# Performance work log

Hardware: AMD Instinct MI355X
Metric: run time of the kernel (lower is better)

The kernel has to match this reference:

```python
import jax, jax.numpy as jnp
import numpy as np

EMBED_DIM = 1024
N_HEADS = 16
HEAD_DIM = EMBED_DIM // N_HEADS


def setup_inputs() -> dict:
    key = jax.random.key(0)
    ks = jax.random.split(key, 9)
    s = 1.0 / np.sqrt(EMBED_DIM)
    x = jax.random.normal(ks[0], (4, 2048, EMBED_DIM), dtype=jnp.float32)
    Wq = jax.random.uniform(ks[1], (EMBED_DIM, EMBED_DIM), jnp.float32, -s, s)
    bq = jax.random.uniform(ks[2], (EMBED_DIM,), jnp.float32, -s, s)
    Wk = jax.random.uniform(ks[3], (EMBED_DIM, EMBED_DIM), jnp.float32, -s, s)
    bk = jax.random.uniform(ks[4], (EMBED_DIM,), jnp.float32, -s, s)
    Wv = jax.random.uniform(ks[5], (EMBED_DIM, EMBED_DIM), jnp.float32, -s, s)
    bv = jax.random.uniform(ks[6], (EMBED_DIM,), jnp.float32, -s, s)
    Wo = jax.random.uniform(ks[7], (EMBED_DIM, EMBED_DIM), jnp.float32, -s, s)
    bo = jax.random.uniform(ks[8], (EMBED_DIM,), jnp.float32, -s, s)
    return {"x": x, "Wq": Wq, "bq": bq, "Wk": Wk, "bk": bk,
            "Wv": Wv, "bv": bv, "Wo": Wo, "bo": bo}


def reference(x, Wq, bq, Wk, bk, Wv, bv, Wo, bo):
    B, S, _ = x.shape
    # projections (PyTorch Linear: x @ W.T + b; weights stored as [in,out] here)
    q = x @ Wq + bq
    k = x @ Wk + bk
    v = x @ Wv + bv
    # [B, H, S, D]
    q = q.reshape(B, S, N_HEADS, HEAD_DIM).transpose(0, 2, 1, 3)
    k = k.reshape(B, S, N_HEADS, HEAD_DIM).transpose(0, 2, 1, 3)
    v = v.reshape(B, S, N_HEADS, HEAD_DIM).transpose(0, 2, 1, 3)
    scores = jnp.einsum('bhsd,bhtd->bhst', q, k) / np.sqrt(HEAD_DIM).astype(np.float32)
    attn = jax.nn.softmax(scores, axis=-1)
    out = jnp.einsum('bhst,bhtd->bhsd', attn, v)
    out = out.transpose(0, 2, 1, 3).reshape(B, S, EMBED_DIM)
    return out @ Wo + bo  # dropout=0 (eval) -> identity
```

## Files before the change

### kernel.cpp

```cpp
#include <hip/hip_runtime.h>
#include <stdint.h>

#define EMBED 1024
#define NH 16
#define HD 64
#define SEQ 2048
#define BATCH 4
#define M_TOT (BATCH*SEQ)
#define QSCALE 0.18033688011112042f

typedef __attribute__((ext_vector_type(8))) short short8;
typedef __attribute__((ext_vector_type(4))) float floatx4;
typedef __attribute__((ext_vector_type(4))) unsigned int uintx4;

__device__ __forceinline__ unsigned short f2bf(float f) {
    union { float f; unsigned int u; } v; v.f = f;
    unsigned int r = v.u + 0x7fffu + ((v.u >> 16) & 1u);
    return (unsigned short)(r >> 16);
}

__device__ __forceinline__ void load_lds16(const unsigned short* g, unsigned short* l) {
    __builtin_amdgcn_global_load_lds(
        (const __attribute__((address_space(1))) unsigned int*)g,
        (__attribute__((address_space(3))) unsigned int*)l, 16, 0, 0);
}

__global__ void cvt_x(const float* __restrict__ x, unsigned short* __restrict__ xb) {
    int i = (blockIdx.x * 256 + threadIdx.x) * 4;
    float4 v = *(const float4*)(x + i);
    ushort4 o;
    o.x = f2bf(v.x); o.y = f2bf(v.y); o.z = f2bf(v.z); o.w = f2bf(v.w);
    *(ushort4*)(xb + i) = o;
}

__global__ void wtrans(const float* __restrict__ w0, const float* __restrict__ w1,
                       const float* __restrict__ w2, const float* __restrict__ w3,
                       unsigned short* __restrict__ t0, unsigned short* __restrict__ t1,
                       unsigned short* __restrict__ t2, unsigned short* __restrict__ t3) {
    __shared__ float tile[32][33];
    const float* W; unsigned short* T;
    switch (blockIdx.z) { case 0: W=w0; T=t0; break; case 1: W=w1; T=t1; break;
                          case 2: W=w2; T=t2; break; default: W=w3; T=t3; }
    int n0 = blockIdx.x * 32, k0 = blockIdx.y * 32;
    int tx = threadIdx.x, ty = threadIdx.y;
    #pragma unroll
    for (int i = 0; i < 4; i++)
        tile[ty + i*8][tx] = W[(k0 + ty + i*8) * EMBED + n0 + tx];
    __syncthreads();
    #pragma unroll
    for (int i = 0; i < 4; i++)
        T[(n0 + ty + i*8) * EMBED + k0 + tx] = f2bf(tile[tx][ty + i*8]);
}

__global__ __launch_bounds__(256) void gemm_st(
        const unsigned short* __restrict__ A, const unsigned short* __restrict__ BT,
        const float* __restrict__ b0, const float* __restrict__ b1, const float* __restrict__ b2,
        void* __restrict__ o0, void* __restrict__ o1, void* __restrict__ o2, int mode) {
    __shared__ unsigned short As[128*32];
    __shared__ unsigned short Bs[128*32];
    int tid = threadIdx.x;
    int lane = tid & 63, wave = tid >> 6;
    int quad = lane >> 4, l16 = lane & 15;
    int id = blockIdx.x;
    int xcd = id & 7, j = id >> 3;
    int mblk = (xcd * 8 + (j & 7)) * 128;
    int nblk = (j >> 3) * 128;
    int wm = wave >> 1, wn = wave & 1;
    floatx4 acc[4][4];
    #pragma unroll
    for (int mt=0;mt<4;mt++)
      #pragma unroll
      for (int nt=0;nt<4;nt++)
        acc[mt][nt] = (floatx4){0.f,0.f,0.f,0.f};
    int lr = lane >> 2;
    int lc = ((lane & 3) ^ ((lr >> 1) & 3)) * 8;
    const unsigned short* Ag = A  + (size_t)(mblk + wave*32 + lr) * EMBED + lc;
    const unsigned short* Bg = BT + (size_t)(nblk + wave*32 + lr) * EMBED + lc;
    unsigned short* Asw = As + wave*1024;
    unsigned short* Bsw = Bs + wave*1024;
    int sa = (quad ^ ((l16 >> 1) & 3)) * 8;

    for (int k0 = 0; k0 < EMBED; k0 += 32) {
        load_lds16(Ag + k0,             Asw);
        load_lds16(Ag + 16*EMBED + k0,  Asw + 512);
        load_lds16(Bg + k0,             Bsw);
        load_lds16(Bg + 16*EMBED + k0,  Bsw + 512);
        __syncthreads();
        short8 af[4], bf[4];
        #pragma unroll
        for (int i=0;i<4;i++) {
            af[i] = *(const short8*)(As + (wm*64 + i*16 + l16)*32 + sa);
            bf[i] = *(const short8*)(Bs + (wn*64 + i*16 + l16)*32 + sa);
        }
        #pragma unroll
        for (int mt=0;mt<4;mt++)
          #pragma unroll
          for (int nt=0;nt<4;nt++)
            acc[mt][nt] = __builtin_amdgcn_mfma_f32_16x16x32_bf16(af[mt], bf[nt], acc[mt][nt], 0, 0, 0);
        __syncthreads();
    }
    if (mode == 1) {
        float* O = (float*)o0;
        #pragma unroll
        for (int mt=0;mt<4;mt++)
          #pragma unroll
          for (int nt=0;nt<4;nt++) {
            int col = nblk + wn*64 + nt*16 + l16;
            float bv = b0[col];
            #pragma unroll
            for (int r=0;r<4;r++) {
                int row = mblk + wm*64 + mt*16 + quad*4 + r;
                O[(size_t)row * EMBED + col] = acc[mt][nt][r] + bv;
            }
          }
    } else {
        int which = (nblk + wn*64) >> 10;
        const float* bs = (which==0) ? b0 : (which==1) ? b1 : b2;
        unsigned short* O = (unsigned short*)((which==0) ? o0 : (which==1) ? o1 : o2);
        #pragma unroll
        for (int mt=0;mt<4;mt++)
          #pragma unroll
          for (int nt=0;nt<4;nt++) {
            int coll = ((nblk + wn*64) & 1023) + nt*16 + l16;
            float bv = bs[coll];
            int h = coll >> 6, d = coll & 63;
            #pragma unroll
            for (int r=0;r<4;r++) {
                int row = mblk + wm*64 + mt*16 + quad*4 + r;
                int b = row >> 11, s = row & 2047;
                float v = acc[mt][nt][r] + bv;
                if (which == 0) {
                    v *= QSCALE;
                    O[((size_t)(b*NH + h)*SEQ + s)*HD + d] = f2bf(v);
                } else if (which == 1) {
                    O[((size_t)(b*NH + h)*SEQ + s)*HD + d] = f2bf(v);
                } else {
                    int sp = (s & ~31) | (((s >> 2) & 3) << 3) | (((s >> 4) & 1) << 2) | (s & 3);
                    O[((size_t)(b*NH + h)*HD + d)*SEQ + sp] = f2bf(v);
                }
            }
          }
    }
}

__global__ __launch_bounds__(512, 4) void attn(
    const unsigned short* __restrict__ Q, const unsigned short* __restrict__ K,
    const unsigned short* __restrict__ VTp, unsigned short* __restrict__ O) {
    __shared__ unsigned short kv[4096];
    int tid = threadIdx.x;
    int lane = tid & 63, wave = tid >> 6;
    int quad = lane >> 4, l16 = lane & 15;
    int id = blockIdx.x;
    int bh = (id & 7) * 8 + (id >> 6);
    int qblk = (id >> 3) & 7;
    int b = bh >> 4, h = bh & 15;
    int q0 = qblk * 256 + wave * 32;
    const unsigned short* Qb = Q + (size_t)bh * SEQ * HD;
    const unsigned short* Kb = K + (size_t)bh * SEQ * HD;
    const unsigned short* Vb = VTp + (size_t)bh * HD * SEQ;
    int li = (wave & 3) * 64 + lane;
    const unsigned short* src;
    unsigned short* dst = kv + (wave & 3) * 512 + ((wave >> 2) ? 2048 : 0);
    int src_step;
    if (wave < 4) {
        int t = li >> 3, slot = li & 7;
        int dblk = slot ^ (t & 7);
        src = Kb + (size_t)t * HD + dblk * 8;
        src_step = 32 * HD;
    } else {
        int d = li >> 2, slot = li & 3;
        int swz = (d & 3) ^ ((d >> 2) & 3);
        src = Vb + (size_t)d * SEQ + (slot ^ swz) * 8;
        src_step = 32;
    }
    short8 qf[2][2];
    #pragma unroll
    for (int mt=0;mt<2;mt++) {
        const unsigned short* qp = Qb + (size_t)(q0 + mt*16 + l16) * HD + quad*8;
        qf[mt][0] = *(const short8*)(qp);
        qf[mt][1] = *(const short8*)(qp + 32);
    }
    floatx4 o_acc[2][4], l_acc[2];
    #pragma unroll
    for (int mt=0;mt<2;mt++) {
        l_acc[mt] = (floatx4){0.f,0.f,0.f,0.f};
        #pragma unroll
        for (int dt=0;dt<4;dt++) o_acc[mt][dt] = (floatx4){0.f,0.f,0.f,0.f};
    }
    short8 ones;
    #pragma unroll
    for (int j=0;j<8;j++) ones[j] = (short)0x3F80;
    int koff[2][2], voff[4];
    #pragma unroll
    for (int nt=0;nt<2;nt++) {
        int t = nt*16 + l16;
        #pragma unroll
        for (int hh=0;hh<2;hh++)
            koff[nt][hh] = t*64 + ((hh*4 + quad) ^ (t & 7)) * 8;
    }
    #pragma unroll
    for (int dt=0;dt<4;dt++) {
        int d = dt*16 + l16;
        voff[dt] = 2048 + d*32 + ((quad ^ (d & 3) ^ ((d >> 2) & 3))) * 8;
    }

    for (int tb = 0; tb < SEQ; tb += 32) {
        load_lds16(src, dst);
        src += src_step;
        __syncthreads();
        short8 kf[2][2], vf[4];
        #pragma unroll
        for (int nt=0;nt<2;nt++) {
            kf[nt][0] = *(const short8*)(kv + koff[nt][0]);
            kf[nt][1] = *(const short8*)(kv + koff[nt][1]);
        }
        #pragma unroll
        for (int dt=0;dt<4;dt++)
            vf[dt] = *(const short8*)(kv + voff[dt]);
        floatx4 sacc[2][2];
        #pragma unroll
        for (int nt=0;nt<2;nt++)
          #pragma unroll
          for (int mt=0;mt<2;mt++) {
            floatx4 s = (floatx4){0.f,0.f,0.f,0.f};
            s = __builtin_amdgcn_mfma_f32_16x16x32_bf16(kf[nt][0], qf[mt][0], s, 0, 0, 0);
            s = __builtin_amdgcn_mfma_f32_16x16x32_bf16(kf[nt][1], qf[mt][1], s, 0, 0, 0);
            sacc[nt][mt] = s;
          }
        short8 pf[2];
        #pragma unroll
        for (int mt=0;mt<2;mt++) {
            uintx4 pu;
            #pragma unroll
            for (int jp=0;jp<4;jp++) {
                int nt = jp >> 1, rp = (jp & 1) * 2;
                union { float f; unsigned int u; } e0, e1;
                e0.f = __builtin_amdgcn_exp2f(sacc[nt][mt][rp]);
                e1.f = __builtin_amdgcn_exp2f(sacc[nt][mt][rp+1]);
                pu[jp] = ((e1.u + 0x8000u) & 0xFFFF0000u) | ((e0.u + 0x8000u) >> 16);
            }
            pf[mt] = __builtin_bit_cast(short8, pu);
        }
        #pragma unroll
        for (int mt=0;mt<2;mt++) {
            l_acc[mt] = __builtin_amdgcn_mfma_f32_16x16x32_bf16(ones, pf[mt], l_acc[mt], 0, 0, 0);
            #pragma unroll
            for (int dt=0;dt<4;dt++)
                o_acc[mt][dt] = __builtin_amdgcn_mfma_f32_16x16x32_bf16(vf[dt], pf[mt], o_acc[mt][dt], 0, 0, 0);
        }
        __syncthreads();
    }
    #pragma unroll
    for (int mt=0;mt<2;mt++) {
        float inv = 1.f / l_acc[mt][0];
        int s = q0 + mt*16 + l16;
        #pragma unroll
        for (int dt=0;dt<4;dt++) {
            ushort4 w;
            w.x = f2bf(o_acc[mt][dt][0]*inv);
            w.y = f2bf(o_acc[mt][dt][1]*inv);
            w.z = f2bf(o_acc[mt][dt][2]*inv);
            w.w = f2bf(o_acc[mt][dt][3]*inv);
            *(ushort4*)(O + ((size_t)b*SEQ + s)*EMBED + h*HD + dt*16 + quad*4) = w;
        }
    }
}

extern "C" void kernel_launch(void* const* d_in, const int* in_sizes, int n_in,
                              void* d_out, int out_size, void* d_ws, size_t ws_size,
                              hipStream_t stream) {
    const float* x  = (const float*)d_in[0];
    const float* Wq = (const float*)d_in[1]; const float* bq = (const float*)d_in[2];
    const float* Wk = (const float*)d_in[3]; const float* bk = (const float*)d_in[4];
    const float* Wv = (const float*)d_in[5]; const float* bv = (const float*)d_in[6];
    const float* Wo = (const float*)d_in[7]; const float* bo = (const float*)d_in[8];
    char* ws = (char*)d_ws;
    unsigned short* xb  = (unsigned short*)(ws);
    unsigned short* WqT = (unsigned short*)(ws + (16ull<<20));
    unsigned short* WkT = (unsigned short*)(ws + (18ull<<20));
    unsigned short* WvT = (unsigned short*)(ws + (20ull<<20));
    unsigned short* WoT = (unsigned short*)(ws + (22ull<<20));
    unsigned short* Qb  = (unsigned short*)(ws + (24ull<<20));
    unsigned short* Kb  = (unsigned short*)(ws + (40ull<<20));
    unsigned short* VTb = (unsigned short*)(ws + (56ull<<20));
    unsigned short* Ob  = xb;

    cvt_x<<<(M_TOT*EMBED)/1024, 256, 0, stream>>>(x, xb);
    wtrans<<<dim3(32,32,4), dim3(32,8), 0, stream>>>(Wq,Wk,Wv,Wo, WqT,WkT,WvT,WoT);
    gemm_st<<<dim3(1536), 256, 0, stream>>>(xb, WqT, bq, bk, bv, Qb, Kb, VTb, 0);
    attn<<<dim3(512), 512, 0, stream>>>(Qb, Kb, VTb, Ob);
    gemm_st<<<dim3(512), 256, 0, stream>>>(Ob, WoT, bo, bo, bo, (float*)d_out, nullptr, nullptr, 1);
}
```

Baseline: 289.6 us.

## Replace projection GEMM with 256x256 double-buffered eight-wave pipelined kernel

```diff
diff --git a/kernel.cpp b/kernel.cpp
--- a/kernel.cpp
+++ b/kernel.cpp
@@ -52,81 +52,164 @@
         T[(n0 + ty + i*8) * EMBED + k0 + tx] = f2bf(tile[tx][ty + i*8]);
 }
 
-__global__ __launch_bounds__(256) void gemm_st(
+#define ST_A(buf_, kt_) do { \
+    const unsigned short* s_ = Asrc + (kt_)*64; \
+    unsigned short* d_ = ldst + (buf_)*32768; \
+    load_lds16(s_,              d_); \
+    load_lds16(s_ + 64*EMBED,   d_ + 4096); \
+    load_lds16(s_ + 128*EMBED,  d_ + 8192); \
+    load_lds16(s_ + 192*EMBED,  d_ + 12288); \
+  } while(0)
+#define ST_B(buf_, kt_, h_) do { \
+    const unsigned short* s_ = Bsrc + (kt_)*64 + (h_)*128*EMBED; \
+    unsigned short* d_ = ldst + (buf_)*32768 + 16384 + (h_)*8192; \
+    load_lds16(s_,              d_); \
+    load_lds16(s_ + 64*EMBED,   d_ + 4096); \
+  } while(0)
+
+__global__ __launch_bounds__(512, 2) void gemm8(
         const unsigned short* __restrict__ A, const unsigned short* __restrict__ BT,
         const float* __restrict__ b0, const float* __restrict__ b1, const float* __restrict__ b2,
         void* __restrict__ o0, void* __restrict__ o1, void* __restrict__ o2, int mode) {
-    __shared__ unsigned short As[128*32];
-    __shared__ unsigned short Bs[128*32];
-    int tid = threadIdx.x;
-    int lane = tid & 63, wave = tid >> 6;
-    int quad = lane >> 4, l16 = lane & 15;
-    int id = blockIdx.x;
-    int xcd = id & 7, j = id >> 3;
-    int mblk = (xcd * 8 + (j & 7)) * 128;
-    int nblk = (j >> 3) * 128;
-    int wm = wave >> 1, wn = wave & 1;
-    floatx4 acc[4][4];
-    #pragma unroll
-    for (int mt=0;mt<4;mt++)
+    __shared__ unsigned short lds[2][2][256*64];
+    const int tid = threadIdx.x;
+    const int lane = tid & 63, wave = tid >> 6;
+    const int quad = lane >> 4, l16 = lane & 15;
+    const int wm = wave >> 2, wn = wave & 3;
+    const int id = blockIdx.x;
+    const int xcd = id & 7, j = id >> 3;
+    const int mblk = (xcd * 4 + (j & 3)) * 256;
+    const int nblk = (j >> 2) * 256;
+
+    const int srow = tid >> 3;
+    const int scol = ((tid & 7) ^ (srow & 7)) * 8;
+    const unsigned short* Asrc = A  + (size_t)(mblk + srow) * EMBED + scol;
+    const unsigned short* Bsrc = BT + (size_t)(nblk + srow) * EMBED + scol;
+    unsigned short* ldst = &lds[0][0][0] + wave * 512;
+
+    const int cs0 = ( quad      ^ (l16 & 7)) * 8;
+    const int cs1 = ((quad ^ 4) ^ (l16 & 7)) * 8;
+    const unsigned short* Abase = &lds[0][0][0] + (wm*128 + l16)*64;
+    const unsigned short* Bbase = &lds[0][1][0] + (wn*64  + l16)*64;
+
+    floatx4 acc[8][4];
+    #pragma unroll
+    for (int m=0;m<8;m++)
       #pragma unroll
-      for (int nt=0;nt<4;nt++)
-        acc[mt][nt] = (floatx4){0.f,0.f,0.f,0.f};
-    int lr = lane >> 2;
-    int lc = ((lane & 3) ^ ((lr >> 1) & 3)) * 8;
-    const unsigned short* Ag = A  + (size_t)(mblk + wave*32 + lr) * EMBED + lc;
-    const unsigned short* Bg = BT + (size_t)(nblk + wave*32 + lr) * EMBED + lc;
-    unsigned short* Asw = As + wave*1024;
-    unsigned short* Bsw = Bs + wave*1024;
-    int sa = (quad ^ ((l16 >> 1) & 3)) * 8;
-
-    for (int k0 = 0; k0 < EMBED; k0 += 32) {
-        load_lds16(Ag + k0,             Asw);
-        load_lds16(Ag + 16*EMBED + k0,  Asw + 512);
-        load_lds16(Bg + k0,             Bsw);
-        load_lds16(Bg + 16*EMBED + k0,  Bsw + 512);
-        __syncthreads();
-        short8 af[4], bf[4];
+      for (int n=0;n<4;n++) acc[m][n] = (floatx4){0.f,0.f,0.f,0.f};
+
+    ST_A(0,0); ST_B(0,0,0); ST_B(0,0,1);
+    ST_A(1,1);
+    asm volatile("s_waitcnt vmcnt(4)" ::: "memory");
+    __builtin_amdgcn_s_barrier();
+
+    #pragma unroll 2
+    for (int t = 0; t < 16; ++t) {
+        const int buf = t & 1;
+        const unsigned short* Ab = Abase + buf*32768;
+        const unsigned short* Bb = Bbase + buf*32768;
+        short8 fA[4][2], fBlo[2][2], fBhi[2][2];
         #pragma unroll
         for (int i=0;i<4;i++) {
-            af[i] = *(const short8*)(As + (wm*64 + i*16 + l16)*32 + sa);
-            bf[i] = *(const short8*)(Bs + (wn*64 + i*16 + l16)*32 + sa);
-        }
-        #pragma unroll
-        for (int mt=0;mt<4;mt++)
-          #pragma unroll
-          for (int nt=0;nt<4;nt++)
-            acc[mt][nt] = __builtin_amdgcn_mfma_f32_16x16x32_bf16(af[mt], bf[nt], acc[mt][nt], 0, 0, 0);
-        __syncthreads();
-    }
+            fA[i][0] = *(const short8*)(Ab + i*1024 + cs0);
+            fA[i][1] = *(const short8*)(Ab + i*1024 + cs1);
+        }
+        #pragma unroll
+        for (int n=0;n<2;n++) {
+            fBlo[n][0] = *(const short8*)(Bb + n*1024 + cs0);
+            fBlo[n][1] = *(const short8*)(Bb + n*1024 + cs1);
+        }
+        if (t < 15) ST_B(buf^1, t+1, 0);
+        __builtin_amdgcn_s_barrier();
+        asm volatile("s_waitcnt lgkmcnt(0)");
+        __builtin_amdgcn_s_setprio(1);
+        #pragma unroll
+        for (int m=0;m<4;m++)
+          #pragma unroll
+          for (int n=0;n<2;n++) {
+            acc[m][n] = __builtin_amdgcn_mfma_f32_16x16x32_bf16(fA[m][0], fBlo[n][0], acc[m][n], 0,0,0);
+            acc[m][n] = __builtin_amdgcn_mfma_f32_16x16x32_bf16(fA[m][1], fBlo[n][1], acc[m][n], 0,0,0);
+          }
+        __builtin_amdgcn_s_setprio(0);
+        __builtin_amdgcn_s_barrier();
+        #pragma unroll
+        for (int n=0;n<2;n++) {
+            fBhi[n][0] = *(const short8*)(Bb + (2+n)*1024 + cs0);
+            fBhi[n][1] = *(const short8*)(Bb + (2+n)*1024 + cs1);
+        }
+        if (t < 15) ST_B(buf^1, t+1, 1);
+        __builtin_amdgcn_s_barrier();
+        asm volatile("s_waitcnt lgkmcnt(0)");
+        __builtin_amdgcn_s_setprio(1);
+        #pragma unroll
+        for (int m=0;m<4;m++)
+          #pragma unroll
+          for (int n=0;n<2;n++) {
+            acc[m][2+n] = __builtin_amdgcn_mfma_f32_16x16x32_bf16(fA[m][0], fBhi[n][0], acc[m][2+n], 0,0,0);
+            acc[m][2+n] = __builtin_amdgcn_mfma_f32_16x16x32_bf16(fA[m][1], fBhi[n][1], acc[m][2+n], 0,0,0);
+          }
+        __builtin_amdgcn_s_setprio(0);
+        __builtin_amdgcn_s_barrier();
+        #pragma unroll
+        for (int i=0;i<4;i++) {
+            fA[i][0] = *(const short8*)(Ab + (4+i)*1024 + cs0);
+            fA[i][1] = *(const short8*)(Ab + (4+i)*1024 + cs1);
+        }
+        __builtin_amdgcn_s_barrier();
+        asm volatile("s_waitcnt lgkmcnt(0)");
+        __builtin_amdgcn_s_setprio(1);
+        #pragma unroll
+        for (int m=0;m<4;m++)
+          #pragma unroll
+          for (int n=0;n<2;n++) {
+            acc[4+m][2+n] = __builtin_amdgcn_mfma_f32_16x16x32_bf16(fA[m][0], fBhi[n][0], acc[4+m][2+n], 0,0,0);
+            acc[4+m][2+n] = __builtin_amdgcn_mfma_f32_16x16x32_bf16(fA[m][1], fBhi[n][1], acc[4+m][2+n], 0,0,0);
+          }
+        __builtin_amdgcn_s_setprio(0);
+        __builtin_amdgcn_s_barrier();
+        if (t < 14) ST_A(buf, t+2);
+        __builtin_amdgcn_s_setprio(1);
+        #pragma unroll
+        for (int m=0;m<4;m++)
+          #pragma unroll
+          for (int n=0;n<2;n++) {
+            acc[4+m][n] = __builtin_amdgcn_mfma_f32_16x16x32_bf16(fA[m][0], fBlo[n][0], acc[4+m][n], 0,0,0);
+            acc[4+m][n] = __builtin_amdgcn_mfma_f32_16x16x32_bf16(fA[m][1], fBlo[n][1], acc[4+m][n], 0,0,0);
+          }
+        __builtin_amdgcn_s_setprio(0);
+        if (t < 14)       { asm volatile("s_waitcnt vmcnt(4)" ::: "memory"); }
+        else if (t == 14) { asm volatile("s_waitcnt vmcnt(0)" ::: "memory"); }
+        __builtin_amdgcn_s_barrier();
+    }
+
     if (mode == 1) {
         float* O = (float*)o0;
         #pragma unroll
-        for (int mt=0;mt<4;mt++)
+        for (int mt=0;mt<8;mt++)
           #pragma unroll
           for (int nt=0;nt<4;nt++) {
             int col = nblk + wn*64 + nt*16 + l16;
             float bv = b0[col];
             #pragma unroll
             for (int r=0;r<4;r++) {
-                int row = mblk + wm*64 + mt*16 + quad*4 + r;
+                int row = mblk + wm*128 + mt*16 + quad*4 + r;
                 O[(size_t)row * EMBED + col] = acc[mt][nt][r] + bv;
             }
           }
     } else {
-        int which = (nblk + wn*64) >> 10;
+        int which = nblk >> 10;
         const float* bs = (which==0) ? b0 : (which==1) ? b1 : b2;
         unsigned short* O = (unsigned short*)((which==0) ? o0 : (which==1) ? o1 : o2);
         #pragma unroll
-        for (int mt=0;mt<4;mt++)
+        for (int mt=0;mt<8;mt++)
           #pragma unroll
           for (int nt=0;nt<4;nt++) {
-            int coll = ((nblk + wn*64) & 1023) + nt*16 + l16;
+            int coll = (nblk & 1023) + wn*64 + nt*16 + l16;
             float bv = bs[coll];
             int h = coll >> 6, d = coll & 63;
             #pragma unroll
             for (int r=0;r<4;r++) {
-                int row = mblk + wm*64 + mt*16 + quad*4 + r;
+                int row = mblk + wm*128 + mt*16 + quad*4 + r;
                 int b = row >> 11, s = row & 2047;
                 float v = acc[mt][nt][r] + bv;
                 if (which == 0) {
@@ -189,7 +272,7 @@
     }
     short8 ones;
     #pragma unroll
-    for (int j=0;j<8;j++) ones[j] = (short)0x3F80;
+    for (int jj=0;jj<8;jj++) ones[jj] = (short)0x3F80;
     int koff[2][2], voff[4];
     #pragma unroll
     for (int nt=0;nt<2;nt++) {
@@ -287,7 +370,7 @@
 
     cvt_x<<<(M_TOT*EMBED)/1024, 256, 0, stream>>>(x, xb);
     wtrans<<<dim3(32,32,4), dim3(32,8), 0, stream>>>(Wq,Wk,Wv,Wo, WqT,WkT,WvT,WoT);
-    gemm_st<<<dim3(1536), 256, 0, stream>>>(xb, WqT, bq, bk, bv, Qb, Kb, VTb, 0);
+    gemm8<<<dim3(384), 512, 0, stream>>>(xb, WqT, bq, bk, bv, Qb, Kb, VTb, 0);
     attn<<<dim3(512), 512, 0, stream>>>(Qb, Kb, VTb, Ob);
-    gemm_st<<<dim3(512), 256, 0, stream>>>(Ob, WoT, bo, bo, bo, (float*)d_out, nullptr, nullptr, 1);
-}
+    gemm8<<<dim3(128), 512, 0, stream>>>(Ob, WoT, bo, bo, bo, (float*)d_out, nullptr, nullptr, 1);
+}
```

New measurement: 296.8 us. 2.5% more time.
